# Optimization experiments

Measured on AMD Instinct MI355X. Metric: run time of the kernel, lower is better.

## Reference

```python
import jax, jax.numpy as jnp
import numpy as np


def setup_inputs() -> dict:
    key = jax.random.key(0)
    k1, k2 = jax.random.split(key)
    x = jax.random.normal(k1, (16, 128, 64, 64), dtype=jnp.float32)
    # weight layout: [out_channels, in_channels, kh, kw], kernel must be 3 for the
    # original Python-loop bounds to match the allocated output size
    weight = jax.random.normal(k2, (256, 128, 3, 3), dtype=jnp.float32) * 0.05
    return {"x": x, "weight": weight}


def reference(x, weight):
    # Stride-1 conv2d with symmetric zero padding=1 (forward ignores bias/stride/
    # dilation/groups in the original module).
    pad = 1
    out = jax.lax.conv_general_dilated(
        x, weight,
        window_strides=(1, 1),
        padding=[(pad, pad), (pad, pad)],
        dimension_numbers=("NCHW", "OIHW", "NCHW"),
    )
    return out
```

## Files before the change

### kernel.cpp

```cpp
#include <hip/hip_runtime.h>
#include <hip/hip_bf16.h>
#include <stdint.h>

typedef short bf16x8 __attribute__((ext_vector_type(8)));
typedef float f32x4 __attribute__((ext_vector_type(4)));

#define N_IMG 16
#define C_IN  128
#define H_IMG 64
#define W_IMG 64
#define K_OUT 256

#define XB_BYTES (16ull*66*66*128*2)
#define WB_BYTES (9ull*256*128*2)
#define WS_NEED  (XB_BYTES + WB_BYTES)

#define SWZ(L) ((L) ^ ((((L) >> 7) & 3) << 4))

__device__ __forceinline__ void gload16(void* lds, const void* g) {
    __builtin_amdgcn_global_load_lds(
        (const __attribute__((address_space(1))) void*)g,
        (__attribute__((address_space(3))) void*)lds, 16, 0, 0);
}

__global__ void transform_w_kernel(const float* __restrict__ w,
                                   __hip_bfloat16* __restrict__ wb) {
    __shared__ float lw[1152];
    const int kg = blockIdx.x;
    const int t  = threadIdx.x;
    for (int e = t; e < 1152; e += 256) lw[e] = w[kg * 1152 + e];
    __syncthreads();
    for (int e = t; e < 1152; e += 256) {
        int tap = e >> 7;
        int c   = e & 127;
        wb[(tap * 256 + kg) * 128 + c] = __float2bfloat16(lw[c * 9 + tap]);
    }
}

__global__ void transform_x_kernel(const float* __restrict__ x,
                                   __hip_bfloat16* __restrict__ xb) {
    __shared__ uint16_t xsT[64 * 130];
    const int b  = blockIdx.x;
    const int yt = b % 66;
    const int n  = b / 66;
    const int t  = threadIdx.x;
    const bool interior_row = (yt >= 1 && yt <= 64);

    if (interior_row) {
        const float* src = x + (size_t)n * 524288 + (size_t)(yt - 1) * 64;
        for (int e = t; e < 8192; e += 256) {
            int c = e >> 6, gx = e & 63;
            __hip_bfloat16 h = __float2bfloat16(src[c * 4096 + gx]);
            xsT[gx * 130 + c] = *(const uint16_t*)&h;
        }
    }
    __syncthreads();

    uint4* dst = (uint4*)((char*)xb + ((size_t)(n * 66 + yt)) * 66 * 256);
    for (int ch = t; ch < 1056; ch += 256) {
        int xt = ch >> 4;
        int c0 = (ch & 15) * 8;
        uint4 val = make_uint4(0u, 0u, 0u, 0u);
        if (interior_row && xt >= 1 && xt <= 64) {
            const uint16_t* p = &xsT[(xt - 1) * 130 + c0];
            val.x = (uint32_t)p[0] | ((uint32_t)p[1] << 16);
            val.y = (uint32_t)p[2] | ((uint32_t)p[3] << 16);
            val.z = (uint32_t)p[4] | ((uint32_t)p[5] << 16);
            val.w = (uint32_t)p[6] | ((uint32_t)p[7] << 16);
        }
        dst[ch] = val;
    }
}

__global__ __launch_bounds__(256, 3)
void conv3x3_mfma_kernel(const __hip_bfloat16* __restrict__ xbh,
                         const __hip_bfloat16* __restrict__ wbh,
                         float* __restrict__ out) {
    __shared__ uint4 smem[3096];
    char* lds = (char*)smem;
    const char* xg = (const char*)xbh;
    const char* wg = (const char*)wbh;

    const int t  = threadIdx.x;
    const int b  = blockIdx.x;
    const int kt = b & 3;
    const int y  = (b >> 2) & 63;
    const int n  = b >> 8;

    const int lane = t & 63;
    const int wv   = t >> 6;
    const int wr   = wv >> 1;
    const int wc   = wv & 1;
    const int lm   = lane & 15;
    const int g    = lane >> 4;

    const int kbase = wr * 32;
    const int xbase = wc * 32;

    f32x4 acc[2][2];
    #pragma unroll
    for (int i = 0; i < 2; ++i)
        #pragma unroll
        for (int j = 0; j < 2; ++j)
            acc[i][j] = (f32x4){0.f, 0.f, 0.f, 0.f};

    for (int cc = 0; cc < 4; ++cc) {
        for (int ch = t; ch < 792; ch += 256) {
            int sc   = ch ^ ((ch >> 3) & 3);
            int coct = sc & 3;
            int xl   = sc >> 2;
            int row  = xl / 66;
            int xt   = xl - row * 66;
            const char* src = xg + (((size_t)(n * 66 + y + row) * 66 + xt) * 256
                                    + cc * 64 + coct * 16);
            gload16(lds + ch * 16, src);
        }
        for (int ch = t; ch < 2304; ch += 256) {
            int sc   = ch ^ ((ch >> 3) & 3);
            int coct = sc & 3;
            int k    = (sc >> 2) & 63;
            int tap  = sc >> 8;
            const char* src = wg + ((size_t)(tap * 256 + kt * 64 + k) * 256
                                    + cc * 64 + coct * 16);
            gload16(lds + 792 * 16 + ch * 16, src);
        }
        __syncthreads();

        const char* xsb = lds;
        const char* wsb = lds + 792 * 16;
        #pragma unroll
        for (int r = 0; r < 3; ++r) {
            #pragma unroll
            for (int s = 0; s < 3; ++s) {
                const int tap = r * 3 + s;
                int LA0 = (tap * 64 + kbase + 0  + lm) * 64 + g * 16;
                int LA1 = (tap * 64 + kbase + 16 + lm) * 64 + g * 16;
                bf16x8 a0 = *(const bf16x8*)(wsb + SWZ(LA0));
                bf16x8 a1 = *(const bf16x8*)(wsb + SWZ(LA1));
                int xl0 = r * 66 + xbase + s + lm;
                int LB0 = (xl0 * 64)        + g * 16;
                int LB1 = ((xl0 + 16) * 64) + g * 16;
                bf16x8 b0 = *(const bf16x8*)(xsb + SWZ(LB0));
                bf16x8 b1 = *(const bf16x8*)(xsb + SWZ(LB1));
                acc[0][0] = __builtin_amdgcn_mfma_f32_16x16x32_bf16(a0, b0, acc[0][0], 0, 0, 0);
                acc[0][1] = __builtin_amdgcn_mfma_f32_16x16x32_bf16(a0, b1, acc[0][1], 0, 0, 0);
                acc[1][0] = __builtin_amdgcn_mfma_f32_16x16x32_bf16(a1, b0, acc[1][0], 0, 0, 0);
                acc[1][1] = __builtin_amdgcn_mfma_f32_16x16x32_bf16(a1, b1, acc[1][1], 0, 0, 0);
            }
        }
        __syncthreads();
    }

    #pragma unroll
    for (int m = 0; m < 2; ++m) {
        #pragma unroll
        for (int nn = 0; nn < 2; ++nn) {
            const int xcol = xbase + nn * 16 + lm;
            #pragma unroll
            for (int r4 = 0; r4 < 4; ++r4) {
                int k = kt * 64 + kbase + m * 16 + g * 4 + r4;
                out[(((size_t)(n * 256 + k)) * 64 + y) * 64 + xcol] = acc[m][nn][r4];
            }
        }
    }
}

__global__ __launch_bounds__(256, 3)
void conv3x3_f32_kernel(const float* __restrict__ x,
                        const float* __restrict__ w,
                        float* __restrict__ out) {
    __shared__ float xs[16][3][72];
    __shared__ float ws[16][9][64];

    const int t  = threadIdx.x;
    const int kt = blockIdx.x & 3;
    const int y  = (blockIdx.x >> 2) & 63;
    const int n  = blockIdx.x >> 8;

    const int k2   = t >> 3;
    const int xg   = t & 7;
    const int kloc = k2 * 2;
    const int x0   = xg * 8;

    float acc0[8] = {0.f,0.f,0.f,0.f,0.f,0.f,0.f,0.f};
    float acc1[8] = {0.f,0.f,0.f,0.f,0.f,0.f,0.f,0.f};

    const int k0 = kt * 64;

    for (int c0 = 0; c0 < C_IN; c0 += 16) {
        for (int idx = t; idx < 16 * 3 * 66; idx += 256) {
            int col = idx % 66;
            int rc  = idx / 66;
            int r   = rc % 3;
            int c   = rc / 3;
            int gx  = col - 1;
            int gy  = y - 1 + r;
            float v = 0.f;
            if ((unsigned)gx < (unsigned)W_IMG && (unsigned)gy < (unsigned)H_IMG)
                v = x[(((n * C_IN) + c0 + c) * H_IMG + gy) * W_IMG + gx];
            xs[c][r][col] = v;
        }
        for (int idx = t; idx < 64 * 16 * 9; idx += 256) {
            int tap = idx % 9;
            int ck  = idx / 9;
            int c   = ck % 16;
            int k   = ck / 16;
            ws[c][tap][k] = w[((k0 + k) * C_IN + c0 + c) * 9 + tap];
        }
        __syncthreads();

        #pragma unroll 2
        for (int c = 0; c < 16; ++c) {
            #pragma unroll
            for (int r = 0; r < 3; ++r) {
                float xr[10];
                #pragma unroll
                for (int i = 0; i < 10; ++i) xr[i] = xs[c][r][x0 + i];
                #pragma unroll
                for (int s = 0; s < 3; ++s) {
                    float w0 = ws[c][r * 3 + s][kloc];
                    float w1 = ws[c][r * 3 + s][kloc + 1];
                    #pragma unroll
                    for (int i = 0; i < 8; ++i) {
                        acc0[i] = fmaf(w0, xr[i + s], acc0[i]);
                        acc1[i] = fmaf(w1, xr[i + s], acc1[i]);
                    }
                }
            }
        }
        __syncthreads();
    }

    float* o0 = &out[(((n * K_OUT) + k0 + kloc) * H_IMG + y) * W_IMG + x0];
    float* o1 = o0 + H_IMG * W_IMG;
    #pragma unroll
    for (int i = 0; i < 8; ++i) o0[i] = acc0[i];
    #pragma unroll
    for (int i = 0; i < 8; ++i) o1[i] = acc1[i];
}

extern "C" void kernel_launch(void* const* d_in, const int* in_sizes, int n_in,
                              void* d_out, int out_size, void* d_ws, size_t ws_size,
                              hipStream_t stream) {
    const float* x = (const float*)d_in[0];
    const float* w = (const float*)d_in[1];
    float* out = (float*)d_out;
    (void)in_sizes; (void)n_in; (void)out_size;

    if (ws_size >= WS_NEED) {
        __hip_bfloat16* xb = (__hip_bfloat16*)d_ws;
        __hip_bfloat16* wb = (__hip_bfloat16*)((char*)d_ws + XB_BYTES);
        transform_w_kernel<<<256, 256, 0, stream>>>(w, wb);
        transform_x_kernel<<<16 * 66, 256, 0, stream>>>(x, xb);
        conv3x3_mfma_kernel<<<4096, 256, 0, stream>>>(xb, wb, out);
    } else {
        conv3x3_f32_kernel<<<4096, 256, 0, stream>>>(x, w, out);
    }
}
```

Baseline: 152.4 us.

## Restructure conv MFMA kernel into large tiles with triple-buffered weight pipeline

The conv kernel now gives each block all 256 output channels and 4 output rows of one image, using 512 threads and 32x32x16 bf16 MFMAs. The whole input slab is loaded into LDS once, and weight chunks stream through a 3-deep LDS ring with asynchronous global-to-LDS loads and waitcnt-based barriers. The aim is to cut the repeated input and weight refetching and the per-channel-chunk synchronization of the old small-tile design. The x transform is also vectorized with float4 loads and packed bf16 pairs. Only 256 blocks are launched, which risks underfilling the GPU's compute units, and the large LDS footprint limits occupancy.

```diff
diff --git a/kernel.cpp b/kernel.cpp
--- a/kernel.cpp
+++ b/kernel.cpp
@@ -3,7 +3,7 @@
 #include <stdint.h>
 
 typedef short bf16x8 __attribute__((ext_vector_type(8)));
-typedef float f32x4 __attribute__((ext_vector_type(4)));
+typedef float f32x16 __attribute__((ext_vector_type(16)));
 
 #define N_IMG 16
 #define C_IN  128
@@ -15,7 +15,9 @@
 #define WB_BYTES (9ull*256*128*2)
 #define WS_NEED  (XB_BYTES + WB_BYTES)
 
-#define SWZ(L) ((L) ^ ((((L) >> 7) & 3) << 4))
+#define LDSX_BYTES (6*66*256)
+#define WCH_BYTES  16384
+#define LDS_TOTAL  (LDSX_BYTES + 3*WCH_BYTES)
 
 __device__ __forceinline__ void gload16(void* lds, const void* g) {
     __builtin_amdgcn_global_load_lds(
@@ -37,129 +39,167 @@
     }
 }
 
+__device__ __forceinline__ uint32_t pack2(float a, float b) {
+    __hip_bfloat16 ha = __float2bfloat16(a), hb = __float2bfloat16(b);
+    return (uint32_t)*(uint16_t*)&ha | ((uint32_t)*(uint16_t*)&hb << 16);
+}
+
 __global__ void transform_x_kernel(const float* __restrict__ x,
                                    __hip_bfloat16* __restrict__ xb) {
-    __shared__ uint16_t xsT[64 * 130];
+    __shared__ __align__(16) uint32_t xsT[64 * 68];
     const int b  = blockIdx.x;
     const int yt = b % 66;
     const int n  = b / 66;
     const int t  = threadIdx.x;
-    const bool interior_row = (yt >= 1 && yt <= 64);
-
-    if (interior_row) {
-        const float* src = x + (size_t)n * 524288 + (size_t)(yt - 1) * 64;
-        for (int e = t; e < 8192; e += 256) {
-            int c = e >> 6, gx = e & 63;
-            __hip_bfloat16 h = __float2bfloat16(src[c * 4096 + gx]);
-            xsT[gx * 130 + c] = *(const uint16_t*)&h;
+    const bool interior = (yt >= 1 && yt <= 64);
+
+    if (interior) {
+        const float4* src = (const float4*)(x + (size_t)n * 524288 + (size_t)(yt - 1) * 64);
+        #pragma unroll
+        for (int it = 0; it < 4; ++it) {
+            int e  = t + it * 256;
+            int c2 = e >> 4;
+            int x4 = e & 15;
+            float4 va = src[(2 * c2) * 1024 + x4];
+            float4 vb = src[(2 * c2 + 1) * 1024 + x4];
+            int xr = x4 * 4;
+            xsT[(xr + 0) * 68 + c2] = pack2(va.x, vb.x);
+            xsT[(xr + 1) * 68 + c2] = pack2(va.y, vb.y);
+            xsT[(xr + 2) * 68 + c2] = pack2(va.z, vb.z);
+            xsT[(xr + 3) * 68 + c2] = pack2(va.w, vb.w);
         }
     }
     __syncthreads();
 
-    uint4* dst = (uint4*)((char*)xb + ((size_t)(n * 66 + yt)) * 66 * 256);
+    uint4* dst = (uint4*)((char*)xb + (size_t)(n * 66 + yt) * 66 * 256);
     for (int ch = t; ch < 1056; ch += 256) {
         int xt = ch >> 4;
-        int c0 = (ch & 15) * 8;
+        int cp = ch & 15;
         uint4 val = make_uint4(0u, 0u, 0u, 0u);
-        if (interior_row && xt >= 1 && xt <= 64) {
-            const uint16_t* p = &xsT[(xt - 1) * 130 + c0];
-            val.x = (uint32_t)p[0] | ((uint32_t)p[1] << 16);
-            val.y = (uint32_t)p[2] | ((uint32_t)p[3] << 16);
-            val.z = (uint32_t)p[4] | ((uint32_t)p[5] << 16);
-            val.w = (uint32_t)p[6] | ((uint32_t)p[7] << 16);
-        }
+        if (interior && xt >= 1 && xt <= 64)
+            val = *(const uint4*)&xsT[(xt - 1) * 68 + cp * 4];
         dst[ch] = val;
     }
 }
 
-__global__ __launch_bounds__(256, 3)
-void conv3x3_mfma_kernel(const __hip_bfloat16* __restrict__ xbh,
-                         const __hip_bfloat16* __restrict__ wbh,
+__global__ __launch_bounds__(512, 2)
+void conv3x3_mfma_kernel(const char* __restrict__ xg,
+                         const char* __restrict__ wg,
                          float* __restrict__ out) {
-    __shared__ uint4 smem[3096];
-    char* lds = (char*)smem;
-    const char* xg = (const char*)xbh;
-    const char* wg = (const char*)wbh;
-
-    const int t  = threadIdx.x;
-    const int b  = blockIdx.x;
-    const int kt = b & 3;
-    const int y  = (b >> 2) & 63;
-    const int n  = b >> 8;
-
+    __shared__ uint4 smem[LDS_TOTAL / 16];
+    char* lds  = (char*)smem;
+    char* ldsW = lds + LDSX_BYTES;
+
+    const int t    = threadIdx.x;
+    const int b    = blockIdx.x;
+    const int q    = b & 15;
+    const int n    = b >> 4;
     const int lane = t & 63;
     const int wv   = t >> 6;
-    const int wr   = wv >> 1;
-    const int wc   = wv & 1;
-    const int lm   = lane & 15;
-    const int g    = lane >> 4;
-
-    const int kbase = wr * 32;
-    const int xbase = wc * 32;
-
-    f32x4 acc[2][2];
+    const int lm   = lane & 31;
+    const int hi   = lane >> 5;
+    const int kb   = (wv >> 1) * 64;
+    const int mb   = (wv & 1) * 128;
+
+    int addrW[2][2];
+    #pragma unroll
+    for (int kf = 0; kf < 2; ++kf) {
+        int krow = kb + kf * 32 + lm;
+        #pragma unroll
+        for (int ks = 0; ks < 2; ++ks)
+            addrW[kf][ks] = krow * 64 + ((ks * 32 + hi * 16) ^ ((krow & 3) << 4));
+    }
+    int rc0[4];
+    #pragma unroll
+    for (int f = 0; f < 4; ++f) {
+        int m = mb + f * 32 + lm;
+        rc0[f] = (m >> 6) * 66 + (m & 63);
+    }
+    const int coffX0 = hi * 16;
+
+    const int krow0 = t >> 2;
+    const int woffA = krow0 * 256 + (((t & 3) ^ (krow0 & 3)) << 4);
+
+    const char* xsrc = xg + (size_t)(n * 66 + q * 4) * 66 * 256;
+    for (int ch = t; ch < 6336; ch += 512) {
+        int L = ch * 16;
+        gload16(lds + L, xsrc + (L ^ (((L >> 8) & 7) << 4)));
+    }
+    #pragma unroll
+    for (int jj = 0; jj < 2; ++jj) {
+        const char* s = wg + (jj >> 2) * 65536 + (jj & 3) * 64;
+        char* d = ldsW + jj * WCH_BYTES + t * 16;
+        gload16(d, s + woffA);
+        gload16(d + 8192, s + woffA + 32768);
+    }
+    asm volatile("s_waitcnt vmcnt(2)" ::: "memory");
+    __builtin_amdgcn_sched_barrier(0);
+    __builtin_amdgcn_s_barrier();
+
+    f32x16 acc[2][4];
     #pragma unroll
     for (int i = 0; i < 2; ++i)
         #pragma unroll
-        for (int j = 0; j < 2; ++j)
-            acc[i][j] = (f32x4){0.f, 0.f, 0.f, 0.f};
-
-    for (int cc = 0; cc < 4; ++cc) {
-        for (int ch = t; ch < 792; ch += 256) {
-            int sc   = ch ^ ((ch >> 3) & 3);
-            int coct = sc & 3;
-            int xl   = sc >> 2;
-            int row  = xl / 66;
-            int xt   = xl - row * 66;
-            const char* src = xg + (((size_t)(n * 66 + y + row) * 66 + xt) * 256
-                                    + cc * 64 + coct * 16);
-            gload16(lds + ch * 16, src);
-        }
-        for (int ch = t; ch < 2304; ch += 256) {
-            int sc   = ch ^ ((ch >> 3) & 3);
-            int coct = sc & 3;
-            int k    = (sc >> 2) & 63;
-            int tap  = sc >> 8;
-            const char* src = wg + ((size_t)(tap * 256 + kt * 64 + k) * 256
-                                    + cc * 64 + coct * 16);
-            gload16(lds + 792 * 16 + ch * 16, src);
-        }
-        __syncthreads();
-
-        const char* xsb = lds;
-        const char* wsb = lds + 792 * 16;
-        #pragma unroll
-        for (int r = 0; r < 3; ++r) {
+        for (int j = 0; j < 4; ++j)
+            acc[i][j] = (f32x16)(0.f);
+
+    int bR = 0;
+    int bP = 2;
+    for (int j = 0; j < 36; ++j) {
+        {
+            int jj = j + 2; if (jj >= 36) jj -= 36;
+            int tap2 = jj >> 2, cc2 = jj & 3;
+            const char* s = wg + tap2 * 65536 + cc2 * 64;
+            char* d = ldsW + bP * WCH_BYTES + t * 16;
+            gload16(d, s + woffA);
+            gload16(d + 8192, s + woffA + 32768);
+        }
+        const int tap = j >> 2;
+        const int cc  = j & 3;
+        const int r   = (tap >= 6) ? 2 : (tap >= 3 ? 1 : 0);
+        const int s_  = tap - r * 3;
+        const int rs66 = r * 66 + s_;
+        const char* wbuf = ldsW + bR * WCH_BYTES;
+
+        __builtin_amdgcn_s_setprio(1);
+        #pragma unroll
+        for (int ks = 0; ks < 2; ++ks) {
+            bf16x8 a0 = *(const bf16x8*)(wbuf + addrW[0][ks]);
+            bf16x8 a1 = *(const bf16x8*)(wbuf + addrW[1][ks]);
+            const int co = cc * 64 + ks * 32 + coffX0;
             #pragma unroll
-            for (int s = 0; s < 3; ++s) {
-                const int tap = r * 3 + s;
-                int LA0 = (tap * 64 + kbase + 0  + lm) * 64 + g * 16;
-                int LA1 = (tap * 64 + kbase + 16 + lm) * 64 + g * 16;
-                bf16x8 a0 = *(const bf16x8*)(wsb + SWZ(LA0));
-                bf16x8 a1 = *(const bf16x8*)(wsb + SWZ(LA1));
-                int xl0 = r * 66 + xbase + s + lm;
-                int LB0 = (xl0 * 64)        + g * 16;
-                int LB1 = ((xl0 + 16) * 64) + g * 16;
-                bf16x8 b0 = *(const bf16x8*)(xsb + SWZ(LB0));
-                bf16x8 b1 = *(const bf16x8*)(xsb + SWZ(LB1));
-                acc[0][0] = __builtin_amdgcn_mfma_f32_16x16x32_bf16(a0, b0, acc[0][0], 0, 0, 0);
-                acc[0][1] = __builtin_amdgcn_mfma_f32_16x16x32_bf16(a0, b1, acc[0][1], 0, 0, 0);
-                acc[1][0] = __builtin_amdgcn_mfma_f32_16x16x32_bf16(a1, b0, acc[1][0], 0, 0, 0);
-                acc[1][1] = __builtin_amdgcn_mfma_f32_16x16x32_bf16(a1, b1, acc[1][1], 0, 0, 0);
+            for (int f = 0; f < 4; ++f) {
+                int rc = rc0[f] + rs66;
+                int L  = rc * 256 + (co ^ ((rc & 7) << 4));
+                bf16x8 bfr = *(const bf16x8*)(lds + L);
+                acc[0][f] = __builtin_amdgcn_mfma_f32_32x32x16_bf16(a0, bfr, acc[0][f], 0, 0, 0);
+                acc[1][f] = __builtin_amdgcn_mfma_f32_32x32x16_bf16(a1, bfr, acc[1][f], 0, 0, 0);
             }
         }
-        __syncthreads();
-    }
-
-    #pragma unroll
-    for (int m = 0; m < 2; ++m) {
-        #pragma unroll
-        for (int nn = 0; nn < 2; ++nn) {
-            const int xcol = xbase + nn * 16 + lm;
+        __builtin_amdgcn_s_setprio(0);
+
+        asm volatile("s_waitcnt vmcnt(2)" ::: "memory");
+        __builtin_amdgcn_sched_barrier(0);
+        __builtin_amdgcn_s_barrier();
+
+        bR = (bR == 2) ? 0 : bR + 1;
+        bP = (bP == 2) ? 0 : bP + 1;
+    }
+
+    const int y0 = q * 4;
+    #pragma unroll
+    for (int kf = 0; kf < 2; ++kf) {
+        const int kbase2 = kb + kf * 32 + 4 * hi;
+        #pragma unroll
+        for (int f = 0; f < 4; ++f) {
+            int m  = mb + f * 32 + lm;
+            int yy = m >> 6;
+            int xx = m & 63;
+            float* op = out + (((size_t)(n * 256 + kbase2) * 64) + y0 + yy) * 64 + xx;
             #pragma unroll
-            for (int r4 = 0; r4 < 4; ++r4) {
-                int k = kt * 64 + kbase + m * 16 + g * 4 + r4;
-                out[(((size_t)(n * 256 + k)) * 64 + y) * 64 + xcol] = acc[m][nn][r4];
+            for (int reg = 0; reg < 16; ++reg) {
+                int koff = (reg & 3) + 8 * (reg >> 2);
+                op[(size_t)koff * 4096] = acc[kf][f][reg];
             }
         }
     }
@@ -252,7 +292,7 @@
         __hip_bfloat16* wb = (__hip_bfloat16*)((char*)d_ws + XB_BYTES);
         transform_w_kernel<<<256, 256, 0, stream>>>(w, wb);
         transform_x_kernel<<<16 * 66, 256, 0, stream>>>(x, xb);
-        conv3x3_mfma_kernel<<<4096, 256, 0, stream>>>(xb, wb, out);
+        conv3x3_mfma_kernel<<<256, 512, 0, stream>>>((const char*)xb, (const char*)wb, out);
     } else {
         conv3x3_f32_kernel<<<4096, 256, 0, stream>>>(x, w, out);
     }
```

Result: faster. 135.0 us (-11.4%).
